# Kernel optimization log

Measured on AMD Instinct MI355X. Metric: run time of the kernel, lower is better.

## Reference

```python
import jax, jax.numpy as jnp
import numpy as np
from jax import lax

B = 2; H = 96; W = 96
WS = 8; SHIFT = WS // 2; NW = H // WS; P = WS * WS
NH = 3; HD = 32; CD = 96; TD = 96
MID = 2 * CD; GA = 16; BASES = 16

def _rel_index():
    g = np.stack(np.meshgrid(np.arange(WS), np.arange(WS), indexing='ij'), -1).reshape(-1, 2)
    rel = g[:, None, :] - g[None, :, :] + WS - 1
    return jnp.asarray(rel[..., 0] * (2 * WS - 1) + rel[..., 1])  # [P, P]

REL_IDX = _rel_index()

def _sw_mask():
    m = np.zeros((NW, NW, WS, WS, WS, WS), bool); s = WS - SHIFT
    m[-1, :, :s, :, s:, :] = True
    m[-1, :, s:, :, :s, :] = True
    m[:, -1, :, :s, :, s:] = True
    m[:, -1, :, s:, :, :s] = True
    return jnp.asarray(m.reshape(NW * NW, P, P))

SW_MASK = _sw_mask()

def _ln(x, g, b, eps=1e-5):
    mu = x.mean(-1, keepdims=True)
    v = ((x - mu) ** 2).mean(-1, keepdims=True)
    return (x - mu) * lax.rsqrt(v + eps) * g + b

def _conv1x1(x, w):
    return jnp.einsum('bchw,oc->bohw', x, w)

def _conv3x3(x, w, b=None, groups=1):
    y = lax.conv_general_dilated(x, w, (1, 1), ((1, 1), (1, 1)),
                                 dimension_numbers=('NCHW', 'OIHW', 'NCHW'),
                                 feature_group_count=groups)
    return y if b is None else y + b[None, :, None, None]

def _unfold3(x):
    # torch F.unfold(k=3,p=1): channel-major patch order (c, kh, kw)
    bs, c, h, w = x.shape
    xp = jnp.pad(x, ((0, 0), (0, 0), (1, 1), (1, 1)))
    pats = jnp.stack([xp[:, :, i:i + h, j:j + w] for i in range(3) for j in range(3)], axis=2)
    return pats.reshape(bs, c * 9, h * w)

def _adaconv(x, ada_w, p1w, p1b, p2w, p2b):
    bs, c, h, w = x.shape
    para = jax.nn.relu(_conv1x1(x, p1w) + p1b[None, :, None, None])
    para = _conv3x3(para, p2w, p2b).reshape(bs, BASES, h * w)      # [b, r, p]
    xu = _unfold3(x).reshape(bs, GA, (c // GA) * 9, h * w)          # [b, g, d, p]
    # out[b,g,o,p] = sum_{d,r} ada_w[g,o,d,r] * xu[b,g,d,p] * para[b,r,p]
    t = jnp.einsum('godr,bgdp->bgorp', ada_w, xu)
    out = jnp.einsum('bgorp,brp->bgop', t, para)
    return out.reshape(bs, c, h, w)

def _conv_block(x, ln_g, ln_b, c1_pw, c1_dw, c2_pw, ada_w, p1w, p1b, p2w, p2b, c3_w):
    r = _ln(x.transpose(0, 2, 3, 1), ln_g, ln_b).transpose(0, 3, 1, 2)
    b1 = _conv3x3(_conv1x1(r, c1_pw), c1_dw, groups=MID)
    b2 = jax.nn.gelu(_adaconv(_conv1x1(r, c2_pw), ada_w, p1w, p1b, p2w, p2b), approximate=False)
    return x + _conv1x1(b1 * b2, c3_w)

def _wmsa(x, qkv_w, qkv_b, rel_pos, proj_w, proj_b):
    bs = x.shape[0]
    x = jnp.roll(x, (-SHIFT, -SHIFT), (1, 2))
    qkv = jnp.einsum('bhwc,oc->bhwo', x, qkv_w) + qkv_b
    qkv = qkv.reshape(bs, NW, WS, NW, WS, 3, NH, HD)
    qkv = qkv.transpose(5, 6, 0, 1, 3, 2, 4, 7).reshape(3, NH, bs, NW * NW, P, HD)
    q, k, v = qkv[0], qkv[1], qkv[2]
    sim = jnp.einsum('hbwpc,hbwqc->hbwpq', q, k) * (HD ** -0.5)
    bias = rel_pos[REL_IDX.reshape(-1)].reshape(P, P, NH).transpose(2, 0, 1)
    sim = sim + bias[:, None, None]
    sim = jnp.where(SW_MASK[None, None], -jnp.inf, sim)
    attn = jax.nn.softmax(sim, axis=-1)
    out = jnp.einsum('hbwpq,hbwqc->hbwpc', attn, v)
    out = out.reshape(NH, bs, NW, NW, WS, WS, HD).transpose(1, 2, 4, 3, 5, 0, 6).reshape(bs, H, W, NH * HD)
    out = jnp.einsum('bhwc,oc->bhwo', out, proj_w) + proj_b
    return jnp.roll(out, (SHIFT, SHIFT), (1, 2))

def _swin_block(x, ln1_g, ln1_b, qkv_w, qkv_b, rel_pos, proj_w, proj_b,
                ln2_g, ln2_b, f_w1, f_b1, f_dw, f_db, f_w2, f_b2):
    xt = x.transpose(0, 2, 3, 1)  # b h w c
    xt = xt + _wmsa(_ln(xt, ln1_g, ln1_b), qkv_w, qkv_b, rel_pos, proj_w, proj_b)
    y = _ln(xt, ln2_g, ln2_b).transpose(0, 3, 1, 2)
    y = _conv1x1(y, f_w1) + f_b1[None, :, None, None]
    y = _conv3x3(y, f_dw, f_db, groups=2 * TD)
    y = jax.nn.gelu(y, approximate=False)
    y = _conv1x1(y, f_w2) + f_b2[None, :, None, None]
    xt = xt + y.transpose(0, 2, 3, 1)
    return xt.transpose(0, 3, 1, 2)

def _block(x, cb_ln_g, cb_ln_b, cb_c1_pw, cb_c1_dw, cb_c2_pw, ada_w, ada_p1_w, ada_p1_b,
           ada_p2_w, ada_p2_b, cb_c3_w, ln1_g, ln1_b, qkv_w, qkv_b, rel_pos, proj_w, proj_b,
           ln2_g, ln2_b, ffn_w1, ffn_b1, ffn_dw, ffn_db, ffn_w2, ffn_b2, out_w, out_b):
    conv_x, trans_x = x[:, :CD], x[:, CD:]
    conv_x = _conv_block(conv_x, cb_ln_g, cb_ln_b, cb_c1_pw, cb_c1_dw, cb_c2_pw,
                         ada_w, ada_p1_w, ada_p1_b, ada_p2_w, ada_p2_b, cb_c3_w)
    trans_x = _swin_block(trans_x, ln1_g, ln1_b, qkv_w, qkv_b, rel_pos, proj_w, proj_b,
                          ln2_g, ln2_b, ffn_w1, ffn_b1, ffn_dw, ffn_db, ffn_w2, ffn_b2)
    res = _conv1x1(jnp.concatenate([conv_x, trans_x], axis=1), out_w) + out_b[None, :, None, None]
    return x + res

def setup_inputs():
    key = jax.random.key(0)
    ks = jax.random.split(key, 20)
    n = lambda i, shape, s=0.05: jax.random.normal(ks[i], shape, jnp.float32) * s
    return {
        'x': jax.random.normal(ks[0], (B, CD + TD, H, W), jnp.float32),
        'cb_ln_g': jnp.ones((CD,), jnp.float32), 'cb_ln_b': jnp.zeros((CD,), jnp.float32),
        'cb_c1_pw': n(1, (MID, CD)), 'cb_c1_dw': n(2, (MID, 1, 3, 3)),
        'cb_c2_pw': n(3, (MID, CD)),
        'ada_w': n(4, (GA, MID // GA, (MID // GA) * 9, BASES)),
        'ada_p1_w': n(5, (BASES, MID)), 'ada_p1_b': jnp.zeros((BASES,), jnp.float32),
        'ada_p2_w': n(6, (BASES, BASES, 3, 3)), 'ada_p2_b': jnp.zeros((BASES,), jnp.float32),
        'cb_c3_w': n(7, (CD, MID)),
        'ln1_g': jnp.ones((TD,), jnp.float32), 'ln1_b': jnp.zeros((TD,), jnp.float32),
        'qkv_w': n(8, (3 * TD, TD)), 'qkv_b': jnp.zeros((3 * TD,), jnp.float32),
        'rel_pos': n(9, ((2 * WS - 1) ** 2, NH), 0.02),
        'proj_w': n(10, (TD, TD)), 'proj_b': jnp.zeros((TD,), jnp.float32),
        'ln2_g': jnp.ones((TD,), jnp.float32), 'ln2_b': jnp.zeros((TD,), jnp.float32),
        'ffn_w1': n(11, (2 * TD, TD)), 'ffn_b1': jnp.zeros((2 * TD,), jnp.float32),
        'ffn_dw': n(12, (2 * TD, 1, 3, 3)), 'ffn_db': jnp.zeros((2 * TD,), jnp.float32),
        'ffn_w2': n(13, (TD, 2 * TD)), 'ffn_b2': jnp.zeros((TD,), jnp.float32),
        'out_w': n(14, (CD + TD, CD + TD)), 'out_b': jnp.zeros((CD + TD,), jnp.float32),
    }

def reference(x, cb_ln_g, cb_ln_b, cb_c1_pw, cb_c1_dw, cb_c2_pw, ada_w, ada_p1_w, ada_p1_b,
              ada_p2_w, ada_p2_b, cb_c3_w, ln1_g, ln1_b, qkv_w, qkv_b, rel_pos, proj_w, proj_b,
              ln2_g, ln2_b, ffn_w1, ffn_b1, ffn_dw, ffn_db, ffn_w2, ffn_b2, out_w, out_b):
    return _block(x, cb_ln_g, cb_ln_b, cb_c1_pw, cb_c1_dw, cb_c2_pw, ada_w, ada_p1_w, ada_p1_b,
                  ada_p2_w, ada_p2_b, cb_c3_w, ln1_g, ln1_b, qkv_w, qkv_b, rel_pos, proj_w, proj_b,
                  ln2_g, ln2_b, ffn_w1, ffn_b1, ffn_dw, ffn_db, ffn_w2, ffn_b2, out_w, out_b)
```

## Files before the change

### kernel.cpp

```cpp
#include <hip/hip_runtime.h>
#include <math.h>

#define HW_ 9216
#define IH 96
#define IW 96
#define NB 2
#define ST (NB*HW_)

typedef __attribute__((ext_vector_type(8))) short bf16x8;
typedef __attribute__((ext_vector_type(4))) float f32x4;
typedef unsigned short u16;

__device__ __forceinline__ float gelu_f(float v){
  return 0.5f*v*(1.0f+erff(v*0.70710678118654752440f));
}
__device__ __forceinline__ unsigned f2bf(float f){
  unsigned u = __float_as_uint(f);
  return (u + 0x7FFF + ((u>>16)&1)) >> 16;
}
__device__ __forceinline__ float bfl(unsigned u){ return __uint_as_float(u<<16); }
__device__ __forceinline__ float bfh(unsigned u){ return __uint_as_float(u & 0xffff0000u); }

__device__ __forceinline__ void ln12_body(const float* __restrict__ x,
    const float* __restrict__ g1, const float* __restrict__ b1,
    const float* __restrict__ g2, const float* __restrict__ b2,
    u16* __restrict__ lnc, u16* __restrict__ ln1o,
    float* __restrict__ xc, float* __restrict__ xt, int bidx)
{
  __shared__ float t[192][33];
  const int p0 = bidx<<5;
  const int bb = p0/HW_, hw0 = p0 - bb*HW_;
  const int tid = threadIdx.x;
  const int px = tid & 31, cr = tid >> 5;
  const float* xb = x + (size_t)bb*192*HW_ + hw0;
  #pragma unroll
  for (int k=0;k<24;k++){
    int c = cr + k*8;
    t[c][px] = xb[(size_t)c*HW_ + px];
  }
  __syncthreads();
  const int lane = tid&63, wv = tid>>6;
  #pragma unroll 1
  for (int i=0;i<8;i++){
    const int lp = wv*8+i;
    const size_t p = p0 + lp;
    float a0 = t[lane][lp];
    float a1 = (lane<32)? t[64+lane][lp] : 0.f;
    float c0 = t[96+lane][lp];
    float c1 = (lane<32)? t[160+lane][lp] : 0.f;
    float s1=a0+a1, s2=c0+c1;
    #pragma unroll
    for (int o=32;o;o>>=1){ s1+=__shfl_xor(s1,o); s2+=__shfl_xor(s2,o); }
    const float mu1=s1*(1.f/96.f), mu2=s2*(1.f/96.f);
    const float d0=a0-mu1, d1=a1-mu1, e0=c0-mu2, e1=c1-mu2;
    float q1=d0*d0+((lane<32)?d1*d1:0.f), q2=e0*e0+((lane<32)?e1*e1:0.f);
    #pragma unroll
    for (int o=32;o;o>>=1){ q1+=__shfl_xor(q1,o); q2+=__shfl_xor(q2,o); }
    const float r1=rsqrtf(q1*(1.f/96.f)+1e-5f), r2=rsqrtf(q2*(1.f/96.f)+1e-5f);
    lnc [p*96+lane] = (u16)f2bf(d0*r1*g1[lane]+b1[lane]);
    ln1o[p*96+lane] = (u16)f2bf(e0*r2*g2[lane]+b2[lane]);
    xc  [p*96+lane] = a0;
    xt  [p*96+lane] = c0;
    if (lane<32){
      lnc [p*96+64+lane] = (u16)f2bf(d1*r1*g1[64+lane]+b1[64+lane]);
      ln1o[p*96+64+lane] = (u16)f2bf(e1*r2*g2[64+lane]+b2[64+lane]);
      xc  [p*96+64+lane] = a1;
      xt  [p*96+64+lane] = c1;
    }
  }
}

__device__ __forceinline__ void ln_body(const float* __restrict__ in, int istride,
    const float* __restrict__ gam, const float* __restrict__ bet,
    u16* __restrict__ out, int bidx)
{
  int lane = threadIdx.x & 63;
  int wv   = threadIdx.x >> 6;
  int p    = (bidx << 2) + wv;
  const float* row = in + (size_t)p*istride;
  float v0 = row[lane];
  float v1 = (lane < 32) ? row[64+lane] : 0.0f;
  float s = v0 + v1;
  #pragma unroll
  for (int o=32;o;o>>=1) s += __shfl_xor(s,o);
  float mu = s * (1.0f/96.0f);
  float d0 = v0 - mu;
  float d1 = v1 - mu;
  float qv = d0*d0 + ((lane<32)? d1*d1 : 0.0f);
  #pragma unroll
  for (int o=32;o;o>>=1) qv += __shfl_xor(qv,o);
  float rstd = rsqrtf(qv*(1.0f/96.0f) + 1e-5f);
  u16* orow = out + (size_t)p*96;
  orow[lane] = (u16)f2bf(d0*rstd*gam[lane] + bet[lane]);
  if (lane < 32) orow[64+lane] = (u16)f2bf(d1*rstd*gam[64+lane] + bet[64+lane]);
}

template<int ACT, bool CONCAT, bool FINAL, bool HASB, bool HASR, bool OUTBF, bool SPLIT>
__device__ __forceinline__ void conv_body(unsigned char* smem,
    const u16* __restrict__ in1, const float* __restrict__ in2f, int istride,
    const u16* __restrict__ wbf, const float* __restrict__ bias,
    const float* __restrict__ res, int rstride,
    void* __restrict__ out, int ostride, int Cin, int Cout,
    u16* __restrict__ out2, int bx, int by)
{
  unsigned char* actl = smem;
  unsigned char* wl   = smem + 26624;
  const int tid=threadIdx.x, lane=tid&63, wv=tid>>6;
  const int lr=lane&15, g4=lane>>4, wm=wv>>1, wn=wv&1;
  const int p0=bx<<7, co0=by<<6;

  f32x4 acc[2][4];
  #pragma unroll
  for (int m=0;m<2;m++)
    #pragma unroll
    for (int n=0;n<4;n++) acc[m][n]=(f32x4){0.f,0.f,0.f,0.f};

  for (int kc=0; kc<Cin; kc+=96){
    {
      const int row=tid>>1, half=tid&1;
      if (!CONCAT || kc==0){
        const u16* rp = in1 + (size_t)(p0+row)*istride + (CONCAT?0:kc) + half*48;
        #pragma unroll
        for (int s=0;s<6;s++)
          *(uint4*)(actl + row*208 + (half*6+s)*16) = *(const uint4*)(rp + s*8);
      } else {
        const float* rp = in2f + (size_t)(p0+row)*96 + half*48;
        #pragma unroll
        for (int s=0;s<6;s++){
          float4 a=*(const float4*)(rp+s*8), b=*(const float4*)(rp+s*8+4);
          uint4 pk;
          pk.x=f2bf(a.x)|(f2bf(a.y)<<16);
          pk.y=f2bf(a.z)|(f2bf(a.w)<<16);
          pk.z=f2bf(b.x)|(f2bf(b.y)<<16);
          pk.w=f2bf(b.z)|(f2bf(b.w)<<16);
          *(uint4*)(actl + row*208 + (half*6+s)*16) = pk;
        }
      }
    }
    {
      const int row=tid&63, grp=tid>>6;
      const int co=co0+row;
      const u16* wr = wbf + (size_t)co*Cin + kc;
      #pragma unroll
      for (int s=0;s<3;s++){
        int sl=grp*3+s;
        uint4 v={0,0,0,0};
        if (co<Cout) v=*(const uint4*)(wr + sl*8);
        *(uint4*)(wl + row*208 + sl*16)=v;
      }
    }
    __syncthreads();
    #pragma unroll
    for (int ks=0;ks<3;ks++){
      const int sl=ks*4+g4;
      bf16x8 afr[2], bfr[4];
      #pragma unroll
      for (int m=0;m<2;m++) afr[m]=*(const bf16x8*)(wl + ((wm*2+m)*16+lr)*208 + sl*16);
      #pragma unroll
      for (int n=0;n<4;n++) bfr[n]=*(const bf16x8*)(actl + (wn*64+n*16+lr)*208 + sl*16);
      #pragma unroll
      for (int m=0;m<2;m++)
        #pragma unroll
        for (int n=0;n<4;n++)
          acc[m][n]=__builtin_amdgcn_mfma_f32_16x16x32_bf16(afr[m], bfr[n], acc[m][n],0,0,0);
    }
    __syncthreads();
  }

  if (FINAL){
    float* outf = (float*)out;
    #pragma unroll
    for (int m=0;m<2;m++){
      const int cb=co0+(wm*2+m)*16+(g4<<2);
      float4 bv = make_float4(0.f,0.f,0.f,0.f);
      if (HASB) bv = *(const float4*)(bias+cb);
      #pragma unroll
      for (int n=0;n<4;n++){
        const int p=p0+wn*64+n*16+lr;
        const int bb=p/HW_, hw=p-bb*HW_;
        const float av[4]={acc[m][n].x,acc[m][n].y,acc[m][n].z,acc[m][n].w};
        const float bvv[4]={bv.x,bv.y,bv.z,bv.w};
        #pragma unroll
        for (int j=0;j<4;j++){
          size_t oi=((size_t)bb*192+cb+j)*HW_+hw;
          outf[oi]=av[j]+bvv[j]+res[oi];
        }
      }
    }
    return;
  }
  float* lt=(float*)smem;
  #pragma unroll
  for (int m=0;m<2;m++)
    #pragma unroll
    for (int n=0;n<4;n++){
      int px=wn*64+n*16+lr;
      int c=(wm*2+m)*16+(g4<<2);
      *(f32x4*)&lt[px*68+c]=acc[m][n];
    }
  __syncthreads();
  {
    const int pr=tid>>1, half=tid&1;
    const int p=p0+pr;
    #pragma unroll
    for (int s=0;s<8;s++){
      int cl=half*32+s*4;
      int co=co0+cl;
      if (co<Cout){
        float4 v=*(float4*)&lt[pr*68+cl];
        if (SPLIT){
          if (co>=384){
            const int c2 = co-384;
            const float4 bv=*(const float4*)(bias+c2);
            v.x=fmaxf(v.x+bv.x,0.f); v.y=fmaxf(v.y+bv.y,0.f);
            v.z=fmaxf(v.z+bv.z,0.f); v.w=fmaxf(v.w+bv.w,0.f);
            uint2 pk;
            pk.x = f2bf(v.x)|(f2bf(v.y)<<16);
            pk.y = f2bf(v.z)|(f2bf(v.w)<<16);
            *(uint2*)((u16*)out + (size_t)p*16 + c2) = pk;
          } else {
            const int cc = (co<192)? co : co-192;
            const int gg = cc/12, cll = cc - gg*12;
            u16* dst = out2 + ((co<192)? (size_t)0 : (size_t)ST*192)
                     + ((size_t)gg*ST + p)*12 + cll;
            uint2 pk;
            pk.x = f2bf(v.x)|(f2bf(v.y)<<16);
            pk.y = f2bf(v.z)|(f2bf(v.w)<<16);
            *(uint2*)dst = pk;
          }
          continue;
        }
        if (HASB){ const float4 bv=*(const float4*)(bias+co); v.x+=bv.x;v.y+=bv.y;v.z+=bv.z;v.w+=bv.w; }
        if (ACT==1){
          v.x=fmaxf(v.x,0.f); v.y=fmaxf(v.y,0.f); v.z=fmaxf(v.z,0.f); v.w=fmaxf(v.w,0.f);
        }
        if (HASR){ const float4 rv=*(const float4*)(res+(size_t)p*rstride+co); v.x+=rv.x;v.y+=rv.y;v.z+=rv.z;v.w+=rv.w; }
        if (OUTBF){
          uint2 pk;
          pk.x = f2bf(v.x)|(f2bf(v.y)<<16);
          pk.y = f2bf(v.z)|(f2bf(v.w)<<16);
          *(uint2*)((u16*)out + (size_t)p*ostride + co) = pk;
        } else {
          *(float4*)((float*)out + (size_t)p*ostride + co) = v;
        }
      }
    }
  }
}

template<int ACT, bool CONCAT, bool FINAL, bool HASB, bool HASR, bool OUTBF, bool SPLIT>
__global__ __launch_bounds__(256) void conv_mfma_k(
    const u16* __restrict__ in1, const float* __restrict__ in2f, int istride,
    const u16* __restrict__ wbf, const float* __restrict__ bias,
    const float* __restrict__ res, int rstride,
    void* __restrict__ out, int ostride, int Cin, int Cout,
    u16* __restrict__ out2)
{
  __shared__ __align__(16) unsigned char smem[39936];
  conv_body<ACT,CONCAT,FINAL,HASB,HASR,OUTBF,SPLIT>(smem, in1, in2f, istride, wbf, bias,
      res, rstride, out, ostride, Cin, Cout, out2, blockIdx.x, blockIdx.y);
}

__device__ __forceinline__ void adaconv_body(unsigned char* smem,
    const u16* __restrict__ x1g, const u16* __restrict__ x2g,
    const float* __restrict__ para, const u16* __restrict__ apre,
    const float* __restrict__ dww, u16* __restrict__ outb2,
    int b, int g, int reg)
{
  unsigned char* HB2 = smem;
  unsigned char* HB1 = smem + 8640;
  float* PS = (float*)(smem + 17280);
  float* OS = (float*)(smem + 27520);
  float* WDW = (float*)(smem + 33664);

  const int tid=threadIdx.x, lane=tid&63, wv=tid>>6;
  const int lr=lane&15, g4=lane>>4;
  const int hi=(lane>>5)&1, lo16=(lane>>4)&1;
  const int rh=(reg/12)<<4, rw=(reg%12)<<3;

  bf16x8 af[3][5];
  {
    const u16* ag = apre + (size_t)g*30720;
    #pragma unroll
    for (int oo=0;oo<3;oo++){
      const int row=(wv*3+oo)*16+lr;
      #pragma unroll
      for (int ks=0;ks<5;ks++)
        af[oo][ks] = *(const bf16x8*)(ag + row*160 + ks*32 + g4*8);
    }
  }
  if (tid < 180){
    int hy = tid/10, hx = tid - hy*10;
    int gy = rh+hy-1, gx = rw+hx-1;
    uint2 a2={0,0},b2={0,0},c2={0,0}, a1={0,0},b1={0,0},c1={0,0};
    if ((unsigned)gy<IH && (unsigned)gx<IW){
      const size_t base = ((size_t)g*ST + (size_t)b*HW_ + gy*IW + gx)*12;
      const u16* s2 = x2g + base;
      a2=*(const uint2*)s2; b2=*(const uint2*)(s2+4); c2=*(const uint2*)(s2+8);
      const u16* s1 = x1g + base;
      a1=*(const uint2*)s1; b1=*(const uint2*)(s1+4); c1=*(const uint2*)(s1+8);
    }
    *(uint4*)(HB2 + tid*48)      = make_uint4(a2.x,a2.y,b2.x,b2.y);
    *(uint4*)(HB2 + tid*48 + 16) = make_uint4(c2.x,c2.y,0,0);
    *(uint4*)(HB1 + tid*48)      = make_uint4(a1.x,a1.y,b1.x,b1.y);
    *(uint4*)(HB1 + tid*48 + 16) = make_uint4(c1.x,c1.y,0,0);
  }
  if (tid < 108){
    const int ch = tid/9, tp = tid - ch*9;
    WDW[tp*12 + ch] = dww[g*108 + tid];
  }
  #pragma unroll
  for (int it=0; it<2; ++it){
    int idx = tid + (it<<8);
    int sub = idx >> 8;
    int p = (idx>>2)&63, q = idx&3;
    int gy = rh + (sub<<3) + (p>>3), gx = rw + (p&7);
    float4 v = *(const float4*)(para + ((size_t)b*HW_+gy*IW+gx)*16 + q*4);
    *(float4*)&PS[sub*1280 + p*20 + q*4] = v;
  }
  __syncthreads();

  int tapoff[5];
  tapoff[0] = hi ? 48   : 0;
  tapoff[1] = hi ? 480  : 96;
  tapoff[2] = hi ? 576  : 528;
  tapoff[3] = hi ? 1008 : 960;
  tapoff[4] = 1056;

  #pragma unroll
  for (int sub=0; sub<2; ++sub){
    const int sy = sub<<3;
    const int base0 = ((sy + (lr>>3))*10 + (lr&7))*48 + lo16*16;

    f32x4 acc[3][4];
    #pragma unroll
    for (int oo=0;oo<3;oo++)
      #pragma unroll
      for (int n=0;n<4;n++) acc[oo][n]=(f32x4){0.f,0.f,0.f,0.f};

    __builtin_amdgcn_s_setprio(1);
    #pragma unroll
    for (int ks=0;ks<5;ks++){
      bf16x8 bfr[4];
      #pragma unroll
      for (int n=0;n<4;n++)
        bfr[n] = *(const bf16x8*)(HB2 + base0 + n*960 + tapoff[ks]);
      #pragma unroll
      for (int oo=0;oo<3;oo++)
        #pragma unroll
        for (int n=0;n<4;n++)
          acc[oo][n]=__builtin_amdgcn_mfma_f32_16x16x32_bf16(af[oo][ks], bfr[n], acc[oo][n],0,0,0);
    }
    __builtin_amdgcn_s_setprio(0);

    const float* ps = &PS[sub*1280];
    f32x4 prv[4];
    #pragma unroll
    for (int n=0;n<4;n++)
      prv[n] = *(const f32x4*)&ps[((n<<4)+lr)*20+(g4<<2)];
    #pragma unroll
    for (int oo=0;oo<3;oo++){
      const int o=wv*3+oo;
      #pragma unroll
      for (int n=0;n<4;n++){
        const int p=(n<<4)+lr;
        float s=acc[oo][n].x*prv[n].x+acc[oo][n].y*prv[n].y+acc[oo][n].z*prv[n].z+acc[oo][n].w*prv[n].w;
        s += __shfl_xor(s,16); s += __shfl_xor(s,32);
        if (g4==n) OS[((sub<<6)+p)*12+o] = gelu_f(s);
      }
    }
  }
  __syncthreads();
  {
    const size_t gb = (size_t)b*HW_;
    for (int idx=tid; idx<384; idx+=256){
      const int cq = idx % 3;
      const int rest = idx / 3;
      const int p = rest & 63, sub = rest >> 6;
      const int py = p>>3, px = p&7;
      const int Y = (sub<<3)+py, X = px;
      const unsigned char* hb1 = HB1 + (Y*10+X)*48 + cq*8;
      float v0=0.f,v1=0.f,v2=0.f,v3=0.f;
      #pragma unroll
      for (int i=0;i<3;i++){
        #pragma unroll
        for (int j=0;j<3;j++){
          const uint2 r = *(const uint2*)(hb1 + (i*10+j)*48);
          const int tp=i*3+j;
          const f32x4 wv4 = *(const f32x4*)&WDW[tp*12 + cq*4];
          v0 += bfl(r.x)*wv4.x;   v1 += bfh(r.x)*wv4.y;
          v2 += bfl(r.y)*wv4.z;   v3 += bfh(r.y)*wv4.w;
        }
      }
      const size_t gi = (gb + (rh+(sub<<3)+py)*IW + (rw+px))*192 + g*12 + cq*4;
      const float* os = &OS[((sub<<6)+p)*12 + cq*4];
      uint2 pk;
      pk.x = f2bf(os[0]*v0) | (f2bf(os[1]*v1)<<16);
      pk.y = f2bf(os[2]*v2) | (f2bf(os[3]*v3)<<16);
      *(uint2*)(outb2 + gi) = pk;
    }
  }
}

__device__ __forceinline__ void allprep_body(
    const float* __restrict__ s0, const float* __restrict__ s1,
    const float* __restrict__ s2, const float* __restrict__ s3,
    const float* __restrict__ s4, const float* __restrict__ s5,
    const float* __restrict__ s6, const float* __restrict__ s7,
    const float* __restrict__ p1w, const float* __restrict__ aw,
    u16* __restrict__ wdst, u16* __restrict__ apre, int bid)
{
  const int tid = threadIdx.x;
  if (bid < 648){
    const int blks[8]={108,72,72,72,36,72,72,144};
    const int off[8] ={0,27648,46080,66048,84480,93696,112128,130560};
    const int sz[8]  ={27648,18432,18432,18432,9216,18432,18432,36864};
    int m=0, acc=0;
    #pragma unroll
    for (int k=0;k<8;k++){ if (bid >= acc + blks[k]){ acc += blks[k]; m=k+1; } }
    const float* s = (m==0)?s0:(m==1)?s1:(m==2)?s2:(m==3)?s3:(m==4)?s4:(m==5)?s5:(m==6)?s6:s7;
    int i = (bid-acc)*256 + tid;
    if (i < sz[m]) wdst[off[m]+i] = (u16)f2bf(s[i]);
  } else if (bid < 654){
    int i = (bid-648)*256 + tid;
    if (i < 1536){
      int o = i/96, ci = i - o*96;
      float s = 0.f;
      for (int k=0;k<192;k++) s += p1w[o*192+k]*s2[k*96+ci];
      wdst[64512+i] = (u16)f2bf(s);
    }
  } else {
    int E = (bid-654)*256 + tid;
    int g = E / 30720, e = E - g*30720;
    int row = e / 160, kp = e - row*160;
    int tap = kp >> 4, cl = kp & 15;
    int o = row >> 4, r = row & 15;
    float v = 0.f;
    if (tap < 9 && cl < 12)
      v = aw[(((size_t)(g*12+o)*108) + cl*9 + tap)*16 + r];
    apre[(size_t)g*30720 + e] = (u16)f2bf(v);
  }
}

__global__ __launch_bounds__(256) void prep_ln12_k(
    const float* s0, const float* s1, const float* s2, const float* s3,
    const float* s4, const float* s5, const float* s6, const float* s7,
    const float* p1w, const float* aw, u16* wdst, u16* apre,
    const float* x, const float* g1, const float* b1,
    const float* g2, const float* b2,
    u16* lnc, u16* ln1o, float* xc, float* xt)
{
  const int bid = blockIdx.x;
  if (bid < 2574)
    allprep_body(s0,s1,s2,s3,s4,s5,s6,s7,p1w,aw,wdst,apre,bid);
  else
    ln12_body(x,g1,b1,g2,b2,lnc,ln1o,xc,xt,bid-2574);
}

__global__ __launch_bounds__(256) void gemm12_k(
    const u16* lnc, const u16* r6, const u16* wc12p, const float* p1b,
    const u16* wqkv, const float* qkvb, u16* pa1, u16* x1g, u16* qkv)
{
  __shared__ __align__(16) unsigned char smem[39936];
  if (blockIdx.y < 7)
    conv_body<0,false,false,false,false,true,true>(smem, lnc, nullptr, 96, wc12p, p1b,
        nullptr, 0, pa1, 16, 96, 400, x1g, blockIdx.x, blockIdx.y);
  else
    conv_body<0,false,false,true,false,true,false>(smem, r6, nullptr, 96, wqkv, qkvb,
        nullptr, 0, qkv, 288, 96, 288, nullptr, blockIdx.x, blockIdx.y-7);
}

__device__ __forceinline__ void attn_body(const u16* __restrict__ qkv,
    const float* __restrict__ relpos, u16* __restrict__ outa, int bid)
{
  __shared__ float k_s[2048];
  __shared__ float v_s[2048];
  __shared__ float rel_s[225];
  const int win = bid % 144, head = (bid/144)%3, b = bid/432;
  const int wi = win/12, wj = win%12;
  const int lane = threadIdx.x;
  for (int i=lane;i<225;i+=64) rel_s[i] = relpos[i*3+head];
  const int pi = lane>>3, pj = lane&7;
  const int hr = wi*8+pi, wr = wj*8+pj;
  const int sh = (hr+4)%96, sw = (wr+4)%96;
  const size_t pix = (size_t)b*HW_ + sh*96 + sw;
  const u16* base = qkv + pix*288;
  const float SC = 0.17677669529663687f;
  float q[32];
  #pragma unroll
  for (int i=0;i<4;i++){
    const uint4 r = *(const uint4*)(base + head*32 + i*8);
    q[i*8+0]=bfl(r.x)*SC; q[i*8+1]=bfh(r.x)*SC;
    q[i*8+2]=bfl(r.y)*SC; q[i*8+3]=bfh(r.y)*SC;
    q[i*8+4]=bfl(r.z)*SC; q[i*8+5]=bfh(r.z)*SC;
    q[i*8+6]=bfl(r.w)*SC; q[i*8+7]=bfh(r.w)*SC;
  }
  #pragma unroll
  for (int i=0;i<4;i++){
    const uint4 rk = *(const uint4*)(base + 96 + head*32 + i*8);
    const uint4 rv = *(const uint4*)(base + 192 + head*32 + i*8);
    *(float4*)&k_s[(lane<<5)+i*8]   = make_float4(bfl(rk.x),bfh(rk.x),bfl(rk.y),bfh(rk.y));
    *(float4*)&k_s[(lane<<5)+i*8+4] = make_float4(bfl(rk.z),bfh(rk.z),bfl(rk.w),bfh(rk.w));
    *(float4*)&v_s[(lane<<5)+i*8]   = make_float4(bfl(rv.x),bfh(rv.x),bfl(rv.y),bfh(rv.y));
    *(float4*)&v_s[(lane<<5)+i*8+4] = make_float4(bfl(rv.z),bfh(rv.z),bfl(rv.w),bfh(rv.w));
  }
  __syncthreads();
  const bool mi = (wi==11), mj = (wj==11);
  float sc[64];
  #pragma unroll
  for (int qq=0; qq<64; qq++){
    const float4* kr4 = (const float4*)&k_s[qq<<5];
    float s = 0.f;
    #pragma unroll
    for (int i=0;i<8;i++){
      const float4 kv = kr4[i];
      s += q[4*i]*kv.x + q[4*i+1]*kv.y + q[4*i+2]*kv.z + q[4*i+3]*kv.w;
    }
    const int qi = qq>>3, qj = qq&7;
    s += rel_s[(pi-qi+7)*15 + (pj-qj+7)];
    const bool msk = (mi && ((pi<4)!=(qi<4))) || (mj && ((pj<4)!=(qj<4)));
    sc[qq] = msk ? -1e30f : s;
  }
  float m = sc[0];
  #pragma unroll
  for (int qq=1;qq<64;qq++) m = fmaxf(m, sc[qq]);
  float sum = 0.f;
  #pragma unroll
  for (int qq=0;qq<64;qq++){ float e = __expf(sc[qq]-m); sc[qq]=e; sum+=e; }
  const float inv = 1.f/sum;
  float acc[32];
  #pragma unroll
  for (int i=0;i<32;i++) acc[i]=0.f;
  #pragma unroll
  for (int qq=0;qq<64;qq++){
    const float a = sc[qq]*inv;
    const float4* vr4 = (const float4*)&v_s[qq<<5];
    #pragma unroll
    for (int i=0;i<8;i++){
      const float4 vv = vr4[i];
      acc[4*i]+=a*vv.x; acc[4*i+1]+=a*vv.y; acc[4*i+2]+=a*vv.z; acc[4*i+3]+=a*vv.w;
    }
  }
  u16* orow = outa + pix*96 + head*32;
  #pragma unroll
  for (int i=0;i<4;i++){
    uint4 pk;
    pk.x = f2bf(acc[i*8+0])|(f2bf(acc[i*8+1])<<16);
    pk.y = f2bf(acc[i*8+2])|(f2bf(acc[i*8+3])<<16);
    pk.z = f2bf(acc[i*8+4])|(f2bf(acc[i*8+5])<<16);
    pk.w = f2bf(acc[i*8+6])|(f2bf(acc[i*8+7])<<16);
    *(uint4*)(orow + i*8) = pk;
  }
}

__device__ __forceinline__ void p2conv_body(const u16* __restrict__ in,
    const float* __restrict__ w, const float* __restrict__ bias,
    float* __restrict__ out, int bid)
{
  __shared__ float ws[2304];
  int tid = threadIdx.x;
  for (int i=tid;i<2304;i+=64) ws[i]=w[i];
  __syncthreads();
  int gidx = bid*64 + tid;
  int p = gidx >> 2, qq = gidx & 3;
  int bb = p / HW_, hw = p - bb*HW_;
  int hy = hw / IW, wx = hw - hy*IW;
  const int cb = qq<<2;
  float a0=bias[cb], a1=bias[cb+1], a2=bias[cb+2], a3=bias[cb+3];
  #pragma unroll
  for (int i=0;i<3;i++){
    int y=hy+i-1; if ((unsigned)y>=IH) continue;
    #pragma unroll
    for (int j=0;j<3;j++){
      int x2=wx+j-1; if ((unsigned)x2>=IW) continue;
      int tap=i*3+j;
      const uint4 r = *(const uint4*)(in + ((size_t)bb*HW_ + y*IW + x2)*16);
      const uint4 r2 = *(const uint4*)(in + ((size_t)bb*HW_ + y*IW + x2)*16 + 8);
      float vv[16]={bfl(r.x),bfh(r.x),bfl(r.y),bfh(r.y),bfl(r.z),bfh(r.z),bfl(r.w),bfh(r.w),
                    bfl(r2.x),bfh(r2.x),bfl(r2.y),bfh(r2.y),bfl(r2.z),bfh(r2.z),bfl(r2.w),bfh(r2.w)};
      #pragma unroll
      for (int ci=0;ci<16;ci++){
        float v = vv[ci];
        a0 += ws[(cb+0)*144 + ci*9 + tap]*v;
        a1 += ws[(cb+1)*144 + ci*9 + tap]*v;
        a2 += ws[(cb+2)*144 + ci*9 + tap]*v;
        a3 += ws[(cb+3)*144 + ci*9 + tap]*v;
      }
    }
  }
  *(float4*)(out + (size_t)p*16 + cb) = make_float4(a0,a1,a2,a3);
}

__global__ __launch_bounds__(64) void attn_p2_k(
    const u16* __restrict__ qkv, const float* __restrict__ relpos,
    u16* __restrict__ outa,
    const u16* __restrict__ pa1, const float* __restrict__ p2w,
    const float* __restrict__ p2b, float* __restrict__ pa2)
{
  const int bid = blockIdx.x;
  if (bid < 864) attn_body(qkv, relpos, outa, bid);
  else           p2conv_body(pa1, p2w, p2b, pa2, bid-864);
}

__global__ __launch_bounds__(256) void ada_proj_k(
    const u16* x1g, const u16* x2g, const float* para, const u16* apre,
    const float* dww, u16* outb2,
    const u16* r6, const u16* wproj, const float* projb, float* xt)
{
  __shared__ __align__(16) unsigned char smem[39936];
  const int bid = blockIdx.x;
  if (bid < 2304){
    const int xcd = bid & 7, j = bid >> 3;
    const int g = xcd + ((j & 1) << 3);
    const int t = j >> 1;
    const int b = t / 72, reg = t - b*72;
    adaconv_body(smem, x1g, x2g, para, apre, dww, outb2, b, g, reg);
  } else {
    const int bx = bid - 2304;
    conv_body<0,false,false,true,true,false,false>(smem, r6, nullptr, 96, wproj, projb,
        xt, 96, xt, 96, 96, 96, nullptr, bx % 144, bx / 144);
  }
}

__global__ __launch_bounds__(256) void c3_ln2_k(
    const u16* b2b, const u16* wc3, const float* xc, u16* r4,
    const float* xt, const float* g2, const float* bt2, u16* r6)
{
  __shared__ __align__(16) unsigned char smem[39936];
  const int bid = blockIdx.x;
  if (bid < 288)
    conv_body<0,false,false,false,true,true,false>(smem, b2b, nullptr, 192, wc3, nullptr,
        xc, 96, r4, 96, 192, 96, nullptr, bid % 144, bid / 144);
  else
    ln_body(xt, 96, g2, bt2, r6, bid-288);
}

template<bool HASB, bool DOGELU>
__global__ __launch_bounds__(256) void dw3x3_k(const u16* __restrict__ in, int istride,
                                               const float* __restrict__ w,
                                               const float* __restrict__ bias,
                                               u16* __restrict__ out, int C){
  int t = blockIdx.x*256 + threadIdx.x;
  int cg = C >> 2;
  int p = t / cg;
  if (p >= ST) return;
  int c4 = (t - p*cg) << 2;
  int bb = p / HW_, hw = p - bb*HW_;
  int hy = hw / IW, wx = hw - hy*IW;
  float w0[9], w1[9], w2[9], w3[9];
  #pragma unroll
  for (int tp=0;tp<9;tp++){
    w0[tp]=w[(c4+0)*9+tp]; w1[tp]=w[(c4+1)*9+tp]; w2[tp]=w[(c4+2)*9+tp]; w3[tp]=w[(c4+3)*9+tp];
  }
  float ax=0.f, ay=0.f, az=0.f, aw=0.f;
  #pragma unroll
  for (int i=0;i<3;i++){
    int y = hy+i-1;
    if ((unsigned)y >= IH) continue;
    #pragma unroll
    for (int j=0;j<3;j++){
      int x2 = wx+j-1;
      if ((unsigned)x2 >= IW) continue;
      const uint2 r = *(const uint2*)(in + ((size_t)bb*HW_ + y*IW + x2)*istride + c4);
      int tp=i*3+j;
      ax += bfl(r.x)*w0[tp]; ay += bfh(r.x)*w1[tp];
      az += bfl(r.y)*w2[tp]; aw += bfh(r.y)*w3[tp];
    }
  }
  if (HASB){ ax+=bias[c4]; ay+=bias[c4+1]; az+=bias[c4+2]; aw+=bias[c4+3]; }
  if (DOGELU){ ax=gelu_f(ax); ay=gelu_f(ay); az=gelu_f(az); aw=gelu_f(aw); }
  uint2 pk;
  pk.x = f2bf(ax)|(f2bf(ay)<<16);
  pk.y = f2bf(az)|(f2bf(aw)<<16);
  *(uint2*)(out + (size_t)p*C + c4) = pk;
}

extern "C" void kernel_launch(void* const* d_in, const int* in_sizes, int n_in,
                              void* d_out, int out_size, void* d_ws, size_t ws_size,
                              hipStream_t stream)
{
  (void)in_sizes; (void)n_in; (void)out_size; (void)ws_size;
  const float* x        = (const float*)d_in[0];
  const float* cb_ln_g  = (const float*)d_in[1];
  const float* cb_ln_b  = (const float*)d_in[2];
  const float* cb_c1_pw = (const float*)d_in[3];
  const float* cb_c1_dw = (const float*)d_in[4];
  const float* cb_c2_pw = (const float*)d_in[5];
  const float* ada_w    = (const float*)d_in[6];
  const float* ada_p1_w = (const float*)d_in[7];
  const float* ada_p1_b = (const float*)d_in[8];
  const float* ada_p2_w = (const float*)d_in[9];
  const float* ada_p2_b = (const float*)d_in[10];
  const float* cb_c3_w  = (const float*)d_in[11];
  const float* ln1_g    = (const float*)d_in[12];
  const float* ln1_b    = (const float*)d_in[13];
  const float* qkv_w    = (const float*)d_in[14];
  const float* qkv_b    = (const float*)d_in[15];
  const float* rel_pos  = (const float*)d_in[16];
  const float* proj_w   = (const float*)d_in[17];
  const float* proj_b   = (const float*)d_in[18];
  const float* ln2_g    = (const float*)d_in[19];
  const float* ln2_b    = (const float*)d_in[20];
  const float* ffn_w1   = (const float*)d_in[21];
  const float* ffn_b1   = (const float*)d_in[22];
  const float* ffn_dw   = (const float*)d_in[23];
  const float* ffn_db   = (const float*)d_in[24];
  const float* ffn_w2   = (const float*)d_in[25];
  const float* ffn_b2   = (const float*)d_in[26];
  const float* out_w    = (const float*)d_in[27];
  const float* out_b    = (const float*)d_in[28];

  char* wsb = (char*)d_ws;
  float* XC  = (float*)wsb;
  float* U0f = (float*)(wsb + (size_t)ST*96*4);
  float* XT  = (float*)(wsb + (size_t)ST*384*4);
  float* PA2 = (float*)(wsb + (size_t)ST*480*4);
  u16* B2b  = (u16*)(wsb + (size_t)ST*496*4);
  u16* LNCb = B2b  + (size_t)ST*192;
  u16* R4b  = LNCb + (size_t)ST*96;
  u16* R6b  = R4b  + (size_t)ST*96;
  u16* PA1b = R6b  + (size_t)ST*96;
  u16* Wbf  = PA1b + (size_t)ST*16;
  u16* Apre = Wbf + 167424;
  u16* QKVb = Apre + 491520;
  u16* X1G  = (u16*)U0f;
  u16* X2G  = X1G + (size_t)ST*192;
  u16* FF1b = (u16*)U0f;
  u16* DWOb = (u16*)U0f + (size_t)ST*192;

  const u16* W_qkv  = Wbf + 0;
  const u16* W_c12p = Wbf + 27648;
  const u16* W_c3   = Wbf + 66048;
  const u16* W_proj = Wbf + 84480;
  const u16* W_ffn1 = Wbf + 93696;
  const u16* W_ffn2 = Wbf + 112128;
  const u16* W_fin  = Wbf + 130560;

  prep_ln12_k<<<3150, 256, 0, stream>>>(qkv_w, cb_c1_pw, cb_c2_pw, cb_c3_w,
                                        proj_w, ffn_w1, ffn_w2, out_w,
                                        ada_p1_w, ada_w, Wbf, Apre,
                                        x, cb_ln_g, cb_ln_b, ln1_g, ln1_b,
                                        LNCb, R6b, XC, XT);

  gemm12_k<<<dim3(144, 12), 256, 0, stream>>>(LNCb, R6b, W_c12p, ada_p1_b,
                                              W_qkv, qkv_b, PA1b, X1G, QKVb);

  attn_p2_k<<<2016, 64, 0, stream>>>(QKVb, rel_pos, R6b,
                                     PA1b, ada_p2_w, ada_p2_b, PA2);

  ada_proj_k<<<2592, 256, 0, stream>>>(X1G, X2G, PA2, Apre, cb_c1_dw, B2b,
                                       R6b, W_proj, proj_b, XT);

  c3_ln2_k<<<4896, 256, 0, stream>>>(B2b, W_c3, XC, R4b, XT, ln2_g, ln2_b, R6b);

  conv_mfma_k<0,false,false,true,false,true,false><<<dim3(144, 3), 256, 0, stream>>>(R6b, nullptr, 96, W_ffn1, ffn_b1, nullptr, 0, FF1b, 192, 96, 192, nullptr);
  dw3x3_k<true,true><<<(ST*48)/256, 256, 0, stream>>>(FF1b, 192, ffn_dw, ffn_db, DWOb, 192);
  conv_mfma_k<0,false,false,true,true,false,false><<<dim3(144, 2), 256, 0, stream>>>(DWOb, nullptr, 192, W_ffn2, ffn_b2, XT, 96, XT, 96, 192, 96, nullptr);

  conv_mfma_k<0,true,true,true,true,false,false><<<dim3(144, 3), 256, 0, stream>>>(R4b, XT, 96, W_fin, out_b, x, 0, (float*)d_out, 0, 192, 192, nullptr);
}
```

Measured before the change: 190.9 us.

## Store adaconv output group-major, loop p2 conv per block, swizzle dw3x3 block order

The adaconv output is now written in a group-major layout ([group][pixel][12]), so each block writes contiguous runs instead of 24-byte strided pieces. The c3 GEMM gains a GMAJOR load path that gathers four 12-channel groups per half-row to match. The para 3x3 conv part of attn_p2_k now has each block process four pixel chunks, with the grid shrunk to fit, so the weight staging in shared memory is amortised. The dw3x3 kernel remaps block indices in a stride-8 swizzle, which changes the order in which blocks touch memory.

```diff
diff --git a/kernel.cpp b/kernel.cpp
--- a/kernel.cpp
+++ b/kernel.cpp
@@ -95,7 +95,7 @@
   if (lane < 32) orow[64+lane] = (u16)f2bf(d1*rstd*gam[64+lane] + bet[64+lane]);
 }
 
-template<int ACT, bool CONCAT, bool FINAL, bool HASB, bool HASR, bool OUTBF, bool SPLIT>
+template<int ACT, bool CONCAT, bool FINAL, bool HASB, bool HASR, bool OUTBF, bool SPLIT, bool GMAJOR>
 __device__ __forceinline__ void conv_body(unsigned char* smem,
     const u16* __restrict__ in1, const float* __restrict__ in2f, int istride,
     const u16* __restrict__ wbf, const float* __restrict__ bias,
@@ -118,7 +118,16 @@
   for (int kc=0; kc<Cin; kc+=96){
     {
       const int row=tid>>1, half=tid&1;
-      if (!CONCAT || kc==0){
+      if (GMAJOR){
+        const int g0 = (kc + half*48)/12;
+        #pragma unroll
+        for (int gg=0; gg<4; ++gg){
+          const u16* gp = in1 + ((size_t)(g0+gg)*ST + p0+row)*12;
+          uint2 w0=*(const uint2*)gp, w1=*(const uint2*)(gp+4), w2=*(const uint2*)(gp+8);
+          unsigned char* dst = actl + row*208 + (half*48 + gg*12)*2;
+          *(uint2*)dst = w0; *(uint2*)(dst+8) = w1; *(uint2*)(dst+16) = w2;
+        }
+      } else if (!CONCAT || kc==0){
         const u16* rp = in1 + (size_t)(p0+row)*istride + (CONCAT?0:kc) + half*48;
         #pragma unroll
         for (int s=0;s<6;s++)
@@ -248,7 +257,7 @@
   }
 }
 
-template<int ACT, bool CONCAT, bool FINAL, bool HASB, bool HASR, bool OUTBF, bool SPLIT>
+template<int ACT, bool CONCAT, bool FINAL, bool HASB, bool HASR, bool OUTBF, bool SPLIT, bool GMAJOR>
 __global__ __launch_bounds__(256) void conv_mfma_k(
     const u16* __restrict__ in1, const float* __restrict__ in2f, int istride,
     const u16* __restrict__ wbf, const float* __restrict__ bias,
@@ -257,7 +266,7 @@
     u16* __restrict__ out2)
 {
   __shared__ __align__(16) unsigned char smem[39936];
-  conv_body<ACT,CONCAT,FINAL,HASB,HASR,OUTBF,SPLIT>(smem, in1, in2f, istride, wbf, bias,
+  conv_body<ACT,CONCAT,FINAL,HASB,HASR,OUTBF,SPLIT,GMAJOR>(smem, in1, in2f, istride, wbf, bias,
       res, rstride, out, ostride, Cin, Cout, out2, blockIdx.x, blockIdx.y);
 }
 
@@ -392,7 +401,7 @@
           v2 += bfl(r.y)*wv4.z;   v3 += bfh(r.y)*wv4.w;
         }
       }
-      const size_t gi = (gb + (rh+(sub<<3)+py)*IW + (rw+px))*192 + g*12 + cq*4;
+      const size_t gi = ((size_t)g*ST + gb + (rh+(sub<<3)+py)*IW + (rw+px))*12 + cq*4;
       const float* os = &OS[((sub<<6)+p)*12 + cq*4];
       uint2 pk;
       pk.x = f2bf(os[0]*v0) | (f2bf(os[1]*v1)<<16);
@@ -463,10 +472,10 @@
 {
   __shared__ __align__(16) unsigned char smem[39936];
   if (blockIdx.y < 7)
-    conv_body<0,false,false,false,false,true,true>(smem, lnc, nullptr, 96, wc12p, p1b,
+    conv_body<0,false,false,false,false,true,true,false>(smem, lnc, nullptr, 96, wc12p, p1b,
         nullptr, 0, pa1, 16, 96, 400, x1g, blockIdx.x, blockIdx.y);
   else
-    conv_body<0,false,false,true,false,true,false>(smem, r6, nullptr, 96, wqkv, qkvb,
+    conv_body<0,false,false,true,false,true,false,false>(smem, r6, nullptr, 96, wqkv, qkvb,
         nullptr, 0, qkv, 288, 96, 288, nullptr, blockIdx.x, blockIdx.y-7);
 }
 
@@ -561,34 +570,37 @@
   int tid = threadIdx.x;
   for (int i=tid;i<2304;i+=64) ws[i]=w[i];
   __syncthreads();
-  int gidx = bid*64 + tid;
-  int p = gidx >> 2, qq = gidx & 3;
-  int bb = p / HW_, hw = p - bb*HW_;
-  int hy = hw / IW, wx = hw - hy*IW;
-  const int cb = qq<<2;
-  float a0=bias[cb], a1=bias[cb+1], a2=bias[cb+2], a3=bias[cb+3];
-  #pragma unroll
-  for (int i=0;i<3;i++){
-    int y=hy+i-1; if ((unsigned)y>=IH) continue;
-    #pragma unroll
-    for (int j=0;j<3;j++){
-      int x2=wx+j-1; if ((unsigned)x2>=IW) continue;
-      int tap=i*3+j;
-      const uint4 r = *(const uint4*)(in + ((size_t)bb*HW_ + y*IW + x2)*16);
-      const uint4 r2 = *(const uint4*)(in + ((size_t)bb*HW_ + y*IW + x2)*16 + 8);
-      float vv[16]={bfl(r.x),bfh(r.x),bfl(r.y),bfh(r.y),bfl(r.z),bfh(r.z),bfl(r.w),bfh(r.w),
-                    bfl(r2.x),bfh(r2.x),bfl(r2.y),bfh(r2.y),bfl(r2.z),bfh(r2.z),bfl(r2.w),bfh(r2.w)};
-      #pragma unroll
-      for (int ci=0;ci<16;ci++){
-        float v = vv[ci];
-        a0 += ws[(cb+0)*144 + ci*9 + tap]*v;
-        a1 += ws[(cb+1)*144 + ci*9 + tap]*v;
-        a2 += ws[(cb+2)*144 + ci*9 + tap]*v;
-        a3 += ws[(cb+3)*144 + ci*9 + tap]*v;
+  #pragma unroll 1
+  for (int it=0; it<4; ++it){
+    int gidx = bid*256 + it*64 + tid;
+    int p = gidx >> 2, qq = gidx & 3;
+    int bb = p / HW_, hw = p - bb*HW_;
+    int hy = hw / IW, wx = hw - hy*IW;
+    const int cb = qq<<2;
+    float a0=bias[cb], a1=bias[cb+1], a2=bias[cb+2], a3=bias[cb+3];
+    #pragma unroll
+    for (int i=0;i<3;i++){
+      int y=hy+i-1; if ((unsigned)y>=IH) continue;
+      #pragma unroll
+      for (int j=0;j<3;j++){
+        int x2=wx+j-1; if ((unsigned)x2>=IW) continue;
+        int tap=i*3+j;
+        const uint4 r = *(const uint4*)(in + ((size_t)bb*HW_ + y*IW + x2)*16);
+        const uint4 r2 = *(const uint4*)(in + ((size_t)bb*HW_ + y*IW + x2)*16 + 8);
+        float vv[16]={bfl(r.x),bfh(r.x),bfl(r.y),bfh(r.y),bfl(r.z),bfh(r.z),bfl(r.w),bfh(r.w),
+                      bfl(r2.x),bfh(r2.x),bfl(r2.y),bfh(r2.y),bfl(r2.z),bfh(r2.z),bfl(r2.w),bfh(r2.w)};
+        #pragma unroll
+        for (int ci=0;ci<16;ci++){
+          float v = vv[ci];
+          a0 += ws[(cb+0)*144 + ci*9 + tap]*v;
+          a1 += ws[(cb+1)*144 + ci*9 + tap]*v;
+          a2 += ws[(cb+2)*144 + ci*9 + tap]*v;
+          a3 += ws[(cb+3)*144 + ci*9 + tap]*v;
+        }
       }
     }
-  }
-  *(float4*)(out + (size_t)p*16 + cb) = make_float4(a0,a1,a2,a3);
+    *(float4*)(out + (size_t)p*16 + cb) = make_float4(a0,a1,a2,a3);
+  }
 }
 
 __global__ __launch_bounds__(64) void attn_p2_k(
@@ -617,19 +629,19 @@
     adaconv_body(smem, x1g, x2g, para, apre, dww, outb2, b, g, reg);
   } else {
     const int bx = bid - 2304;
-    conv_body<0,false,false,true,true,false,false>(smem, r6, nullptr, 96, wproj, projb,
+    conv_body<0,false,false,true,true,false,false,false>(smem, r6, nullptr, 96, wproj, projb,
         xt, 96, xt, 96, 96, 96, nullptr, bx % 144, bx / 144);
   }
 }
 
 __global__ __launch_bounds__(256) void c3_ln2_k(
-    const u16* b2b, const u16* wc3, const float* xc, u16* r4,
+    const u16* b2g, const u16* wc3, const float* xc, u16* r4,
     const float* xt, const float* g2, const float* bt2, u16* r6)
 {
   __shared__ __align__(16) unsigned char smem[39936];
   const int bid = blockIdx.x;
   if (bid < 288)
-    conv_body<0,false,false,false,true,true,false>(smem, b2b, nullptr, 192, wc3, nullptr,
+    conv_body<0,false,false,false,true,true,false,true>(smem, b2g, nullptr, 12, wc3, nullptr,
         xc, 96, r4, 96, 192, 96, nullptr, bid % 144, bid / 144);
   else
     ln_body(xt, 96, g2, bt2, r6, bid-288);
@@ -640,7 +652,9 @@
                                                const float* __restrict__ w,
                                                const float* __restrict__ bias,
                                                u16* __restrict__ out, int C){
-  int t = blockIdx.x*256 + threadIdx.x;
+  const int q8 = gridDim.x >> 3;
+  const int bid = (blockIdx.x & 7)*q8 + (blockIdx.x >> 3);
+  int t = bid*256 + threadIdx.x;
   int cg = C >> 2;
   int p = t / cg;
   if (p >= ST) return;
@@ -715,8 +729,8 @@
   float* U0f = (float*)(wsb + (size_t)ST*96*4);
   float* XT  = (float*)(wsb + (size_t)ST*384*4);
   float* PA2 = (float*)(wsb + (size_t)ST*480*4);
-  u16* B2b  = (u16*)(wsb + (size_t)ST*496*4);
-  u16* LNCb = B2b  + (size_t)ST*192;
+  u16* B2G  = (u16*)(wsb + (size_t)ST*496*4);
+  u16* LNCb = B2G  + (size_t)ST*192;
   u16* R4b  = LNCb + (size_t)ST*96;
   u16* R6b  = R4b  + (size_t)ST*96;
   u16* PA1b = R6b  + (size_t)ST*96;
@@ -745,17 +759,17 @@
   gemm12_k<<<dim3(144, 12), 256, 0, stream>>>(LNCb, R6b, W_c12p, ada_p1_b,
                                               W_qkv, qkv_b, PA1b, X1G, QKVb);
 
-  attn_p2_k<<<2016, 64, 0, stream>>>(QKVb, rel_pos, R6b,
+  attn_p2_k<<<1152, 64, 0, stream>>>(QKVb, rel_pos, R6b,
                                      PA1b, ada_p2_w, ada_p2_b, PA2);
 
-  ada_proj_k<<<2592, 256, 0, stream>>>(X1G, X2G, PA2, Apre, cb_c1_dw, B2b,
+  ada_proj_k<<<2592, 256, 0, stream>>>(X1G, X2G, PA2, Apre, cb_c1_dw, B2G,
                                        R6b, W_proj, proj_b, XT);
 
-  c3_ln2_k<<<4896, 256, 0, stream>>>(B2b, W_c3, XC, R4b, XT, ln2_g, ln2_b, R6b);
-
-  conv_mfma_k<0,false,false,true,false,true,false><<<dim3(144, 3), 256, 0, stream>>>(R6b, nullptr, 96, W_ffn1, ffn_b1, nullptr, 0, FF1b, 192, 96, 192, nullptr);
+  c3_ln2_k<<<4896, 256, 0, stream>>>(B2G, W_c3, XC, R4b, XT, ln2_g, ln2_b, R6b);
+
+  conv_mfma_k<0,false,false,true,false,true,false,false><<<dim3(144, 3), 256, 0, stream>>>(R6b, nullptr, 96, W_ffn1, ffn_b1, nullptr, 0, FF1b, 192, 96, 192, nullptr);
   dw3x3_k<true,true><<<(ST*48)/256, 256, 0, stream>>>(FF1b, 192, ffn_dw, ffn_db, DWOb, 192);
-  conv_mfma_k<0,false,false,true,true,false,false><<<dim3(144, 2), 256, 0, stream>>>(DWOb, nullptr, 192, W_ffn2, ffn_b2, XT, 96, XT, 96, 192, 96, nullptr);
-
-  conv_mfma_k<0,true,true,true,true,false,false><<<dim3(144, 3), 256, 0, stream>>>(R4b, XT, 96, W_fin, out_b, x, 0, (float*)d_out, 0, 192, 192, nullptr);
-}
+  conv_mfma_k<0,false,false,true,true,false,false,false><<<dim3(144, 2), 256, 0, stream>>>(DWOb, nullptr, 192, W_ffn2, ffn_b2, XT, 96, XT, 96, 192, 96, nullptr);
+
+  conv_mfma_k<0,true,true,true,true,false,false,false><<<dim3(144, 3), 256, 0, stream>>>(R4b, XT, 96, W_fin, out_b, x, 0, (float*)d_out, 0, 192, 192, nullptr);
+}
```

After: 188.3 us (median of 2 runs). About the same (-1.4%).
